# Kernel optimization log

Measured on AMD Instinct MI355X. Metric: run time of the kernel, lower is better.

## Reference

```python
import jax, jax.numpy as jnp
import numpy as np

FEAT_STRIDE = 16
PRE_NMS_TOPN = 6000
POST_NMS_TOPN = 300
NMS_THRESH = 0.7
MIN_SIZE = 16.0
NEG = -1e9


def _whctrs(a):
    w = a[2] - a[0] + 1.0
    h = a[3] - a[1] + 1.0
    return w, h, a[0] + 0.5 * (w - 1), a[1] + 0.5 * (h - 1)


def _mkanchors(ws, hs, xc, yc):
    return np.stack([xc - 0.5 * (ws - 1), yc - 0.5 * (hs - 1),
                     xc + 0.5 * (ws - 1), yc + 0.5 * (hs - 1)], axis=1)


def generate_anchors(base_size=16, ratios=(0.5, 1.0, 2.0), scales=(8, 16, 32)):
    base = np.array([0, 0, base_size - 1, base_size - 1], dtype=np.float64)
    w, h, xc, yc = _whctrs(base)
    size = w * h
    ratios = np.array(ratios, dtype=np.float64)
    ws = np.round(np.sqrt(size / ratios))
    hs = np.round(ws * ratios)
    ratio_anchors = _mkanchors(ws, hs, xc, yc)
    out = []
    for a in ratio_anchors:
        w, h, xc, yc = _whctrs(a)
        s = np.array(scales, dtype=np.float64)
        out.append(_mkanchors(w * s, h * s, xc, yc))
    return np.concatenate(out, axis=0).astype(np.float32)


def _nms_single(boxes, scores):
    # boxes [N,4], scores [N] (sorted desc by top_k); greedy NMS, fixed POST_NMS_TOPN picks
    x1, y1, x2, y2 = boxes[:, 0], boxes[:, 1], boxes[:, 2], boxes[:, 3]
    areas = (x2 - x1 + 1.0) * (y2 - y1 + 1.0)

    def body(i, st):
        keep, ok, live = st
        s = jnp.where(live, scores, NEG - 1.0)
        j = jnp.argmax(s)
        valid = s[j] > NEG / 2
        keep = keep.at[i].set(j.astype(jnp.int32))
        ok = ok.at[i].set(valid)
        xx1 = jnp.maximum(x1[j], x1)
        yy1 = jnp.maximum(y1[j], y1)
        xx2 = jnp.minimum(x2[j], x2)
        yy2 = jnp.minimum(y2[j], y2)
        inter = jnp.maximum(xx2 - xx1 + 1.0, 0.0) * jnp.maximum(yy2 - yy1 + 1.0, 0.0)
        iou = inter / (areas[j] + areas - inter)
        live = live & (iou <= NMS_THRESH)
        return keep, ok, live

    keep0 = jnp.zeros((POST_NMS_TOPN,), jnp.int32)
    ok0 = jnp.zeros((POST_NMS_TOPN,), bool)
    live0 = scores > NEG / 2
    keep, ok, _ = jax.lax.fori_loop(0, POST_NMS_TOPN, body, (keep0, ok0, live0))
    return keep, ok


def _proposals(rpn_cls_prob, rpn_bbox_pred, im_info, anchors):
    B, _, H, W = rpn_cls_prob.shape
    A = anchors.shape[0]
    # fg scores: second half of the 2A channel dim
    scores = rpn_cls_prob[:, A:].transpose(0, 2, 3, 1).reshape(B, -1)          # [B, H*W*A]
    deltas = rpn_bbox_pred.transpose(0, 2, 3, 1).reshape(B, -1, 4)             # [B, H*W*A, 4]
    # shifted anchors over the feature map
    sx = (jnp.arange(W, dtype=jnp.float32)) * FEAT_STRIDE
    sy = (jnp.arange(H, dtype=jnp.float32)) * FEAT_STRIDE
    gx, gy = jnp.meshgrid(sx, sy)                                              # [H, W]
    shifts = jnp.stack([gx.ravel(), gy.ravel(), gx.ravel(), gy.ravel()], 1)    # [K, 4]
    all_anchors = (shifts[:, None, :] + anchors[None, :, :]).reshape(-1, 4)    # [K*A, 4]
    # bbox_transform_inv
    wa = all_anchors[:, 2] - all_anchors[:, 0] + 1.0
    ha = all_anchors[:, 3] - all_anchors[:, 1] + 1.0
    cxa = all_anchors[:, 0] + 0.5 * (wa - 1.0)
    cya = all_anchors[:, 1] + 0.5 * (ha - 1.0)
    dx, dy, dw, dh = deltas[..., 0], deltas[..., 1], deltas[..., 2], deltas[..., 3]
    cx = dx * wa + cxa
    cy = dy * ha + cya
    pw = jnp.exp(dw) * wa
    ph = jnp.exp(dh) * ha
    x1 = cx - 0.5 * (pw - 1.0)
    y1 = cy - 0.5 * (ph - 1.0)
    x2 = cx + 0.5 * (pw - 1.0)
    y2 = cy + 0.5 * (ph - 1.0)
    # clip to image
    imh = im_info[:, 0:1]
    imw = im_info[:, 1:2]
    x1 = jnp.clip(x1, 0.0, imw - 1.0)
    y1 = jnp.clip(y1, 0.0, imh - 1.0)
    x2 = jnp.clip(x2, 0.0, imw - 1.0)
    y2 = jnp.clip(y2, 0.0, imh - 1.0)
    boxes = jnp.stack([x1, y1, x2, y2], axis=-1)                               # [B, N, 4]
    # filter boxes smaller than min_size * im_scale (mask by score)
    min_sz = MIN_SIZE * im_info[:, 2:3]
    keep_m = ((x2 - x1 + 1.0) >= min_sz) & ((y2 - y1 + 1.0) >= min_sz)
    scores = jnp.where(keep_m, scores, NEG)
    # pre-NMS top-k
    scores_top, order = jax.lax.top_k(scores, PRE_NMS_TOPN)                    # [B, 6000]
    boxes_top = jnp.take_along_axis(boxes, order[:, :, None], axis=1)          # [B, 6000, 4]
    # greedy NMS per image
    keep, keep_ok = jax.vmap(_nms_single)(boxes_top, scores_top)               # [B, 300]
    sel = jnp.take_along_axis(boxes_top, keep[:, :, None], axis=1)             # [B, 300, 4]
    sel = jnp.where(keep_ok[:, :, None], sel, 0.0)
    bidx = jnp.broadcast_to(jnp.arange(B, dtype=sel.dtype)[:, None, None], (B, POST_NMS_TOPN, 1))
    return jnp.concatenate([bidx, sel], axis=-1)                               # [B, 300, 5]


def setup_inputs() -> dict:
    key = jax.random.key(0)
    k1, k2 = jax.random.split(key)
    B, H, W, A = 32, 100, 100, 9
    rpn_cls_prob = jax.random.uniform(k1, (B, 2 * A, H, W), dtype=jnp.float32)
    rpn_bbox_pred = jax.random.normal(k2, (B, 4 * A, H, W), dtype=jnp.float32) * 0.2
    im_info = jnp.tile(jnp.array([[1600.0, 1600.0, 1.0]], dtype=jnp.float32), (B, 1))
    anchors = jnp.asarray(generate_anchors(base_size=16, ratios=(0.5, 1.0, 2.0), scales=(8, 16, 32)))
    return {"rpn_cls_prob": rpn_cls_prob, "rpn_bbox_pred": rpn_bbox_pred,
            "im_info": im_info, "anchors": anchors}


def reference(rpn_cls_prob, rpn_bbox_pred, im_info, anchors):
    return _proposals(rpn_cls_prob, rpn_bbox_pred, im_info, anchors)
```

## Files before the change

### kernel.cpp

```cpp
#include <hip/hip_runtime.h>

#define NB 32
#define NA 9
#define FH 100
#define FW 100
#define HWSZ (FH*FW)
#define NANCH (HWSZ*NA)
#define PRE 6000
#define POST 300
#define SORTN 8192
#define NEGV -1000000000.0f
#define NMS_T 0.7f
#define MARGM 1e-6f
#define NCHUNK ((PRE + 63) / 64)
#define WB() __builtin_amdgcn_wave_barrier()
#define NSLICE 11
#define DSLICE 8192

typedef unsigned long long u64;
typedef unsigned int u32;

__device__ __forceinline__ u32 f2sort(float f) {
  u32 u = __float_as_uint(f);
  return (u & 0x80000000u) ? ~u : (u | 0x80000000u);
}

__device__ __forceinline__ float4 decode_box_pm(const float* __restrict__ pred,
                                                const float* __restrict__ anchors,
                                                int b, int a, int hw,
                                                float imw, float imh) {
  int h = hw / FW; int w = hw - h * FW;
  float sx = (float)(w * 16);
  float sy = (float)(h * 16);
  float ax1 = anchors[a*4+0] + sx, ay1 = anchors[a*4+1] + sy;
  float ax2 = anchors[a*4+2] + sx, ay2 = anchors[a*4+3] + sy;
  float wa = ax2 - ax1 + 1.0f, ha = ay2 - ay1 + 1.0f;
  float cxa = ax1 + 0.5f*(wa - 1.0f), cya = ay1 + 0.5f*(ha - 1.0f);
  size_t base = ((size_t)b*36 + a*4)*HWSZ + hw;
  float dx = pred[base];
  float dy = pred[base + HWSZ];
  float dw = pred[base + 2*HWSZ];
  float dh = pred[base + 3*HWSZ];
  float cx = dx*wa + cxa, cy = dy*ha + cya;
  float pw = expf(dw)*wa, ph = expf(dh)*ha;
  float x1 = fminf(fmaxf(cx - 0.5f*(pw - 1.0f), 0.0f), imw - 1.0f);
  float y1 = fminf(fmaxf(cy - 0.5f*(ph - 1.0f), 0.0f), imh - 1.0f);
  float x2 = fminf(fmaxf(cx + 0.5f*(pw - 1.0f), 0.0f), imw - 1.0f);
  float y2 = fminf(fmaxf(cy + 0.5f*(ph - 1.0f), 0.0f), imh - 1.0f);
  return make_float4(x1, y1, x2, y2);
}

__global__ void k_zero(u32* __restrict__ histcnt) {
  int i = blockIdx.x * 1024 + threadIdx.x;
  histcnt[i] = 0;
}

__global__ __launch_bounds__(1024) void k_decode(
    const float* __restrict__ cls,
    const float* __restrict__ pred,
    const float* __restrict__ iminfo,
    const float* __restrict__ anchors,
    u32* __restrict__ scoreg,
    u32* __restrict__ histg) {
  __shared__ u32 hl[4096];
  const int blk = blockIdx.x;
  const int b = blk / NSLICE, s = blk - b * NSLICE;
  const int tid = threadIdx.x;
  for (int j = tid; j < 4096; j += 1024) hl[j] = 0;
  __syncthreads();
  const float imh = iminfo[b*3+0], imw = iminfo[b*3+1], sc = iminfo[b*3+2];
  const float msz = 16.0f * sc;
  #pragma unroll
  for (int r = 0; r < 8; ++r) {
    int j = s * DSLICE + r * 1024 + tid;
    if (j < NANCH) {
      int a = j / HWSZ; int hw = j - a * HWSZ;
      float score = cls[((size_t)b*18 + 9 + a)*HWSZ + hw];
      float4 bx = decode_box_pm(pred, anchors, b, a, hw, imw, imh);
      bool keep = ((bx.z - bx.x + 1.0f) >= msz) && ((bx.w - bx.y + 1.0f) >= msz);
      float sf = keep ? score : NEGV;
      float t = sf * 4096.0f;
      int bin = (t <= 0.0f) ? 0 : ((t >= 4095.0f) ? 4095 : (int)t);
      atomicAdd(&hl[bin], 1u);
      scoreg[(size_t)b * NANCH + j] = f2sort(sf);
    }
  }
  __syncthreads();
  for (int j = tid; j < 4096; j += 1024) {
    u32 v = hl[j];
    if (v) atomicAdd(&histg[b * 4096 + j], v);
  }
}

__device__ __forceinline__ void w0_cut(u32* hist, u32 target, int lane,
                                       int* cutBin) {
  u32 cs = 0;
  int cb = lane * 64;
  for (int i = 0; i < 64; ++i) cs += hist[cb + ((i + lane) & 63)];
  u32 suf = cs;
  #pragma unroll
  for (int d = 1; d < 64; d <<= 1) {
    u32 o = __shfl_down(suf, (unsigned)d, 64);
    suf += (lane < 64 - d) ? o : 0u;
  }
  u64 m1 = __ballot(suf >= target);
  int L = 63 - __clzll(m1);
  u32 nAb = (L < 63) ? (u32)__builtin_amdgcn_readlane((int)suf, L + 1) : 0u;
  u32 fs = hist[L * 64 + lane];
  #pragma unroll
  for (int d = 1; d < 64; d <<= 1) {
    u32 o = __shfl_down(fs, (unsigned)d, 64);
    fs += (lane < 64 - d) ? o : 0u;
  }
  fs += nAb;
  u64 m2 = __ballot(fs >= target);
  int fb = 63 - __clzll(m2);
  *cutBin = L * 64 + fb;
}

__global__ __launch_bounds__(64) void k_cut(const u32* __restrict__ histg,
                                            u32* __restrict__ thrTg,
                                            u32* __restrict__ binStartG,
                                            u32* __restrict__ countG) {
  __shared__ u32 hl[4096];
  const int b = blockIdx.x, lane = threadIdx.x;
  const u32* h = histg + b * 4096;
  for (int i = lane; i < 4096; i += 64) hl[i] = h[i];
  __syncthreads();
  int L;
  w0_cut(hl, PRE, lane, &L);
  u32 running = 0;
  for (int hi = 4095; hi >= L; hi -= 64) {
    int bin = hi - lane;
    u32 c = (bin >= L && bin >= 0) ? hl[bin] : 0u;
    u32 p = c;
    #pragma unroll
    for (int d = 1; d < 64; d <<= 1) {
      u32 o = __shfl_up(p, (unsigned)d, 64);
      if (lane >= d) p += o;
    }
    if (bin >= L && bin >= 0) binStartG[b * 4096 + bin] = running + p - c;
    running += (u32)__builtin_amdgcn_readlane((int)p, 63);
  }
  if (lane == 0) {
    thrTg[b] = f2sort((float)L * (1.0f / 4096.0f));
    countG[b] = running;
  }
}

__global__ __launch_bounds__(1024) void k_scatter(
    const u32* __restrict__ scoreg,
    const u32* __restrict__ thrTg,
    const u32* __restrict__ binStartG,
    u32* __restrict__ binCntG,
    u64* __restrict__ candg,
    float4* __restrict__ boxg,
    const float* __restrict__ pred,
    const float* __restrict__ iminfo,
    const float* __restrict__ anchors) {
  const int blk = blockIdx.x;
  const int b = blk / NSLICE, s = blk - b * NSLICE;
  const int tid = threadIdx.x;
  const u32 thrT = thrTg[b];
  const float imh = iminfo[b*3+0], imw = iminfo[b*3+1];
  const u32* sb = scoreg + (size_t)b * NANCH;
  #pragma unroll
  for (int r = 0; r < 8; ++r) {
    int j = s * DSLICE + r * 1024 + tid;
    if (j < NANCH) {
      u32 sv = sb[j];
      if (sv >= thrT) {
        int a = j / HWSZ; int hw = j - a * HWSZ;
        int i = hw * NA + a;
        float f = __uint_as_float(sv ^ 0x80000000u);
        float t = f * 4096.0f;
        int bin = (t >= 4095.0f) ? 4095 : (int)t;
        u32 pos = binStartG[b * 4096 + bin] + atomicAdd(&binCntG[b * 4096 + bin], 1u);
        if (pos < SORTN) {
          candg[(size_t)b * SORTN + pos] = ((u64)sv << 32) | (u32)(~(u32)i);
          boxg[(size_t)b * SORTN + pos] = decode_box_pm(pred, anchors, b, a, hw, imw, imh);
        }
      }
    }
  }
}

__global__ __launch_bounds__(512) void k_binsort(
    const u32* __restrict__ binStartG,
    const u32* __restrict__ binCntG,
    u64* __restrict__ candg,
    float4* __restrict__ boxg) {
  __shared__ u64 ks[8][512];
  __shared__ u32 ops[8][512];
  __shared__ float4 bs[8][512];
  const int wave = threadIdx.x >> 6, lane = threadIdx.x & 63;
  const int task = blockIdx.x * 8 + wave;
  const int b = task >> 12, bin = task & 4095;
  u32 cnt = binCntG[b * 4096 + bin];
  if (cnt < 2) return;
  u32 base = binStartG[b * 4096 + bin];
  if (base >= SORTN) return;
  u32 m = cnt;
  if (base + m > SORTN) m = SORTN - base;
  u64* seg = candg + (size_t)b * SORTN + base;
  float4* bseg = boxg + (size_t)b * SORTN + base;
  if (m <= 64) {
    u64 v = (lane < (int)m) ? seg[lane] : 0ull;
    u32 op = (u32)lane;
    #pragma unroll
    for (int k = 2; k <= 64; k <<= 1) {
      for (int j = k >> 1; j > 0; j >>= 1) {
        u64 o = __shfl_xor((unsigned long long)v, j, 64);
        u32 oop = __shfl_xor(op, j, 64);
        bool dirD = ((lane & k) == 0);
        bool lower = ((lane & j) == 0);
        bool takeMax = (dirD == lower);
        bool sw = takeMax ? (o > v) : (o < v);
        if (sw) { v = o; op = oop; }
      }
    }
    if (lane < (int)m) seg[lane] = v;
    if (lane < (int)m) {
      float4 bx = bseg[op];
      bseg[lane] = bx;
    }
  } else if (m <= 512) {
    int np = 128; while (np < (int)m) np <<= 1;
    for (int i = lane; i < np; i += 64) {
      ks[wave][i] = (i < (int)m) ? seg[i] : 0ull;
      ops[wave][i] = (u32)i;
    }
    WB();
    for (int k = 2; k <= np; k <<= 1) {
      for (int j = k >> 1; j > 0; j >>= 1) {
        for (int q = lane; q < np/2; q += 64) {
          int i = ((q & ~(j-1)) << 1) | (q & (j-1));
          int x = i | j;
          u64 a0 = ks[wave][i], a1 = ks[wave][x];
          bool up = (i & k) != 0;
          if (up ? (a0 > a1) : (a0 < a1)) {
            ks[wave][i] = a1; ks[wave][x] = a0;
            u32 t = ops[wave][i]; ops[wave][i] = ops[wave][x]; ops[wave][x] = t;
          }
        }
        WB();
      }
    }
    for (int i = lane; i < (int)m; i += 64) bs[wave][i] = bseg[ops[wave][i]];
    WB();
    for (int i = lane; i < (int)m; i += 64) {
      seg[i] = ks[wave][i];
      bseg[i] = bs[wave][i];
    }
  }
}

__global__ __launch_bounds__(512, 1) void k_nms(
    const float4* __restrict__ boxg,
    const u32* __restrict__ countG,
    float* __restrict__ out) {
  __shared__ float4 boxes[NCHUNK * 64];
  __shared__ float4 accB[POST];
  __shared__ float accA[POST];
  __shared__ u64 okm[2][8];
  const int b = blockIdx.x;
  const int tid = threadIdx.x;
  const int wave = tid >> 6, lane = tid & 63;
  int cnt = (int)countG[b]; if (cnt > PRE) cnt = PRE;
  const float4* bg = boxg + (size_t)b * SORTN;
  for (int i = tid; i < NCHUNK * 64; i += 512) boxes[i] = bg[i];
  __syncthreads();

  int nAcc = 0, lc = 0;
  for (int g = 0; g < NCHUNK; ++g) {
    if (nAcc >= POST) break;
    int nliv = cnt - g * 64;
    if (nliv <= 0) break;
    u64 lm = (nliv >= 64) ? ~0ull : ((1ull << nliv) - 1ull);
    float4 bc = boxes[g * 64 + lane];
    float areaC = (bc.z - bc.x + 1.0f) * (bc.w - bc.y + 1.0f);
    bool ok = (lm >> lane) & 1ull;
    for (int t0 = wave; t0 < nAcc; t0 += 128) {
      if (__ballot(ok) == 0ull) break;
      int te = (t0 + 128 < nAcc) ? (t0 + 128) : nAcc;
      #pragma unroll 2
      for (int tt = t0; tt < te; tt += 8) {
        float4 ba = accB[tt];
        float aA = accA[tt];
        float xx1 = fmaxf(ba.x, bc.x);
        float yy1 = fmaxf(ba.y, bc.y);
        float xx2 = fminf(ba.z, bc.z);
        float yy2 = fminf(ba.w, bc.w);
        float inter = fmaxf(xx2 - xx1 + 1.0f, 0.0f) * fmaxf(yy2 - yy1 + 1.0f, 0.0f);
        float un = aA + areaC - inter;
        float prod = NMS_T * un;
        bool sup = inter > prod;
        if (fabsf(inter - prod) <= MARGM * prod)
          sup = (inter / un) > NMS_T;
        ok = ok && !sup;
      }
    }
    u64 wm = __ballot(ok);
    if (lane == 0) okm[lc & 1][wave] = wm;
    __syncthreads();
    u64 mm = okm[lc & 1][0];
    #pragma unroll
    for (int w = 1; w < 8; ++w) mm &= okm[lc & 1][w];
    ++lc;
    bool ok0 = (mm >> lane) & 1ull;
    u64 bal = __ballot(ok0);
    while (bal != 0ull && nAcc < POST) {
      int fl = __ffsll(bal) - 1;
      float ax1 = __int_as_float(__builtin_amdgcn_readlane(__float_as_int(bc.x), fl));
      float ay1 = __int_as_float(__builtin_amdgcn_readlane(__float_as_int(bc.y), fl));
      float ax2 = __int_as_float(__builtin_amdgcn_readlane(__float_as_int(bc.z), fl));
      float ay2 = __int_as_float(__builtin_amdgcn_readlane(__float_as_int(bc.w), fl));
      float aA = (ax2 - ax1 + 1.0f) * (ay2 - ay1 + 1.0f);
      if (lane == 0) { accB[nAcc] = make_float4(ax1, ay1, ax2, ay2); accA[nAcc] = aA; }
      ++nAcc;
      if (ok0) {
        if (lane == fl) ok0 = false;
        else if (lane > fl) {
          float xx1 = fmaxf(ax1, bc.x);
          float yy1 = fmaxf(ay1, bc.y);
          float xx2 = fminf(ax2, bc.z);
          float yy2 = fminf(ay2, bc.w);
          float inter = fmaxf(xx2 - xx1 + 1.0f, 0.0f) * fmaxf(yy2 - yy1 + 1.0f, 0.0f);
          float iou = inter / (aA + areaC - inter);
          if (iou > NMS_T) ok0 = false;
        }
      }
      bal = __ballot(ok0);
    }
  }

  float* ob = out + (size_t)b * POST * 5;
  for (int i = tid; i < POST * 5; i += 512) {
    int row = i / 5, col = i - row * 5;
    float v = 0.f;
    if (col == 0) v = (float)b;
    else if (row < nAcc) {
      float4 bb = accB[row];
      v = (col == 1) ? bb.x : (col == 2) ? bb.y : (col == 3) ? bb.z : bb.w;
    }
    ob[i] = v;
  }
}

extern "C" void kernel_launch(void* const* d_in, const int* in_sizes, int n_in,
                              void* d_out, int out_size, void* d_ws, size_t ws_size,
                              hipStream_t stream) {
  const float* cls     = (const float*)d_in[0];
  const float* pred    = (const float*)d_in[1];
  const float* iminfo  = (const float*)d_in[2];
  const float* anchors = (const float*)d_in[3];
  float* out = (float*)d_out;

  char* ws = (char*)d_ws;
  u32* histg     = (u32*)(ws + 0);
  u32* binCntG   = (u32*)(ws + 524288);
  u32* binStartG = (u32*)(ws + 1048576);
  u32* thrTg     = (u32*)(ws + 1572864);
  u32* countG    = (u32*)(ws + 1572992);
  u64* candg     = (u64*)(ws + 1573120);
  float4* boxg   = (float4*)(ws + 3670272);
  u32* scoreg    = (u32*)(ws + 7864576);

  k_zero<<<256, 1024, 0, stream>>>(histg);
  k_decode<<<NB*NSLICE, 1024, 0, stream>>>(cls, pred, iminfo, anchors, scoreg, histg);
  k_cut<<<NB, 64, 0, stream>>>(histg, thrTg, binStartG, countG);
  k_scatter<<<NB*NSLICE, 1024, 0, stream>>>(scoreg, thrTg, binStartG, binCntG,
                                            candg, boxg, pred, iminfo, anchors);
  k_binsort<<<16384, 512, 0, stream>>>(binStartG, binCntG, candg, boxg);
  k_nms<<<NB, 512, 0, stream>>>(boxg, countG, out);
}
```

Baseline: 209.0 us.

## Widen NMS to 1024 threads with two candidate chunks per round and cheaper IoU test

The NMS kernel now uses 16 waves and handles two 64-candidate chunks per round, halving the number of block-wide synchronisation rounds. The suppression test is rewritten as a multiply-compare against precomputed 0.7*area terms, with an exact division only inside a narrow tolerance band. The zeroing kernel is replaced with a memset. The greedy accept loop now also has to check the second chunk against each newly accepted box, which adds serial work per round.

```diff
diff --git a/kernel.cpp b/kernel.cpp
--- a/kernel.cpp
+++ b/kernel.cpp
@@ -11,8 +11,9 @@
 #define SORTN 8192
 #define NEGV -1000000000.0f
 #define NMS_T 0.7f
-#define MARGM 1e-6f
+#define BANDR 4e-6f
 #define NCHUNK ((PRE + 63) / 64)
+#define NROUND 47
 #define WB() __builtin_amdgcn_wave_barrier()
 #define NSLICE 11
 #define DSLICE 8192
@@ -48,11 +49,6 @@
   float x2 = fminf(fmaxf(cx + 0.5f*(pw - 1.0f), 0.0f), imw - 1.0f);
   float y2 = fminf(fmaxf(cy + 0.5f*(ph - 1.0f), 0.0f), imh - 1.0f);
   return make_float4(x1, y1, x2, y2);
-}
-
-__global__ void k_zero(u32* __restrict__ histcnt) {
-  int i = blockIdx.x * 1024 + threadIdx.x;
-  histcnt[i] = 0;
 }
 
 __global__ __launch_bounds__(1024) void k_decode(
@@ -255,87 +251,155 @@
   }
 }
 
-__global__ __launch_bounds__(512, 1) void k_nms(
+__global__ __launch_bounds__(1024, 1) void k_nms(
     const float4* __restrict__ boxg,
     const u32* __restrict__ countG,
     float* __restrict__ out) {
   __shared__ float4 boxes[NCHUNK * 64];
   __shared__ float4 accB[POST];
-  __shared__ float accA[POST];
-  __shared__ u64 okm[2][8];
+  __shared__ float4 accT[POST];
+  __shared__ float accA7[POST];
+  __shared__ float accAr[POST];
+  __shared__ u64 okm[2][16][2];
   const int b = blockIdx.x;
   const int tid = threadIdx.x;
   const int wave = tid >> 6, lane = tid & 63;
   int cnt = (int)countG[b]; if (cnt > PRE) cnt = PRE;
   const float4* bg = boxg + (size_t)b * SORTN;
-  for (int i = tid; i < NCHUNK * 64; i += 512) boxes[i] = bg[i];
+  for (int i = tid; i < NCHUNK * 64; i += 1024) boxes[i] = bg[i];
   __syncthreads();
 
   int nAcc = 0, lc = 0;
-  for (int g = 0; g < NCHUNK; ++g) {
+  for (int g = 0; g < NROUND; ++g) {
     if (nAcc >= POST) break;
-    int nliv = cnt - g * 64;
+    int base0 = g * 128;
+    int nliv = cnt - base0;
     if (nliv <= 0) break;
-    u64 lm = (nliv >= 64) ? ~0ull : ((1ull << nliv) - 1ull);
-    float4 bc = boxes[g * 64 + lane];
-    float areaC = (bc.z - bc.x + 1.0f) * (bc.w - bc.y + 1.0f);
-    bool ok = (lm >> lane) & 1ull;
+    u64 lm0 = (nliv >= 64) ? ~0ull : ((1ull << nliv) - 1ull);
+    int nl1 = nliv - 64;
+    u64 lm1 = (nl1 >= 64) ? ~0ull : ((nl1 <= 0) ? 0ull : ((1ull << nl1) - 1ull));
+    float4 bc0 = boxes[base0 + lane];
+    float4 bc1 = boxes[base0 + 64 + lane];
+    float ar0 = (bc0.z - bc0.x + 1.0f) * (bc0.w - bc0.y + 1.0f);
+    float ar1 = (bc1.z - bc1.x + 1.0f) * (bc1.w - bc1.y + 1.0f);
+    float ca0 = NMS_T * ar0, ca1 = NMS_T * ar1;
+    float cz0 = bc0.z + 1.0f, cw0 = bc0.w + 1.0f;
+    float cz1 = bc1.z + 1.0f, cw1 = bc1.w + 1.0f;
+    bool ok0_ = (lm0 >> lane) & 1ull;
+    bool ok1_ = (lm1 >> lane) & 1ull;
     for (int t0 = wave; t0 < nAcc; t0 += 128) {
-      if (__ballot(ok) == 0ull) break;
+      if (__ballot(ok0_ || ok1_) == 0ull) break;
       int te = (t0 + 128 < nAcc) ? (t0 + 128) : nAcc;
-      #pragma unroll 2
-      for (int tt = t0; tt < te; tt += 8) {
-        float4 ba = accB[tt];
-        float aA = accA[tt];
-        float xx1 = fmaxf(ba.x, bc.x);
-        float yy1 = fmaxf(ba.y, bc.y);
-        float xx2 = fminf(ba.z, bc.z);
-        float yy2 = fminf(ba.w, bc.w);
-        float inter = fmaxf(xx2 - xx1 + 1.0f, 0.0f) * fmaxf(yy2 - yy1 + 1.0f, 0.0f);
-        float un = aA + areaC - inter;
-        float prod = NMS_T * un;
-        bool sup = inter > prod;
-        if (fabsf(inter - prod) <= MARGM * prod)
-          sup = (inter / un) > NMS_T;
-        ok = ok && !sup;
-      }
-    }
-    u64 wm = __ballot(ok);
-    if (lane == 0) okm[lc & 1][wave] = wm;
+      for (int tt = t0; tt < te; tt += 16) {
+        float4 bt = accT[tt];
+        float a7 = accA7[tt];
+        {
+          float xx1 = fmaxf(bt.x, bc0.x);
+          float yy1 = fmaxf(bt.y, bc0.y);
+          float x2p = fminf(bt.z, cz0);
+          float y2p = fminf(bt.w, cw0);
+          float inter = fmaxf(x2p - xx1, 0.0f) * fmaxf(y2p - yy1, 0.0f);
+          float lhs = 1.7f * inter;
+          float rhs = a7 + ca0;
+          bool sup = lhs > rhs;
+          if (fabsf(lhs - rhs) <= BANDR * rhs) {
+            float4 bo = accB[tt];
+            float xr1 = fmaxf(bo.x, bc0.x), yr1 = fmaxf(bo.y, bc0.y);
+            float xr2 = fminf(bo.z, bc0.z), yr2 = fminf(bo.w, bc0.w);
+            float ir = fmaxf(xr2 - xr1 + 1.0f, 0.0f) * fmaxf(yr2 - yr1 + 1.0f, 0.0f);
+            sup = (ir / (accAr[tt] + ar0 - ir)) > NMS_T;
+          }
+          ok0_ = ok0_ && !sup;
+        }
+        {
+          float xx1 = fmaxf(bt.x, bc1.x);
+          float yy1 = fmaxf(bt.y, bc1.y);
+          float x2p = fminf(bt.z, cz1);
+          float y2p = fminf(bt.w, cw1);
+          float inter = fmaxf(x2p - xx1, 0.0f) * fmaxf(y2p - yy1, 0.0f);
+          float lhs = 1.7f * inter;
+          float rhs = a7 + ca1;
+          bool sup = lhs > rhs;
+          if (fabsf(lhs - rhs) <= BANDR * rhs) {
+            float4 bo = accB[tt];
+            float xr1 = fmaxf(bo.x, bc1.x), yr1 = fmaxf(bo.y, bc1.y);
+            float xr2 = fminf(bo.z, bc1.z), yr2 = fminf(bo.w, bc1.w);
+            float ir = fmaxf(xr2 - xr1 + 1.0f, 0.0f) * fmaxf(yr2 - yr1 + 1.0f, 0.0f);
+            sup = (ir / (accAr[tt] + ar1 - ir)) > NMS_T;
+          }
+          ok1_ = ok1_ && !sup;
+        }
+      }
+    }
+    u64 w0 = __ballot(ok0_);
+    u64 w1 = __ballot(ok1_);
+    if (lane == 0) { okm[lc & 1][wave][0] = w0; okm[lc & 1][wave][1] = w1; }
     __syncthreads();
-    u64 mm = okm[lc & 1][0];
+    u64 m0 = okm[lc & 1][0][0], m1 = okm[lc & 1][0][1];
     #pragma unroll
-    for (int w = 1; w < 8; ++w) mm &= okm[lc & 1][w];
+    for (int w = 1; w < 16; ++w) { m0 &= okm[lc & 1][w][0]; m1 &= okm[lc & 1][w][1]; }
     ++lc;
-    bool ok0 = (mm >> lane) & 1ull;
-    u64 bal = __ballot(ok0);
-    while (bal != 0ull && nAcc < POST) {
-      int fl = __ffsll(bal) - 1;
-      float ax1 = __int_as_float(__builtin_amdgcn_readlane(__float_as_int(bc.x), fl));
-      float ay1 = __int_as_float(__builtin_amdgcn_readlane(__float_as_int(bc.y), fl));
-      float ax2 = __int_as_float(__builtin_amdgcn_readlane(__float_as_int(bc.z), fl));
-      float ay2 = __int_as_float(__builtin_amdgcn_readlane(__float_as_int(bc.w), fl));
+    bool k0 = (m0 >> lane) & 1ull;
+    bool k1 = (m1 >> lane) & 1ull;
+    u64 bal0 = __ballot(k0), bal1 = __ballot(k1);
+    while ((bal0 | bal1) != 0ull && nAcc < POST) {
+      bool from0 = (bal0 != 0ull);
+      float ax1, ay1, ax2, ay2;
+      int fl;
+      if (from0) {
+        fl = __ffsll(bal0) - 1;
+        ax1 = __int_as_float(__builtin_amdgcn_readlane(__float_as_int(bc0.x), fl));
+        ay1 = __int_as_float(__builtin_amdgcn_readlane(__float_as_int(bc0.y), fl));
+        ax2 = __int_as_float(__builtin_amdgcn_readlane(__float_as_int(bc0.z), fl));
+        ay2 = __int_as_float(__builtin_amdgcn_readlane(__float_as_int(bc0.w), fl));
+      } else {
+        fl = __ffsll(bal1) - 1;
+        ax1 = __int_as_float(__builtin_amdgcn_readlane(__float_as_int(bc1.x), fl));
+        ay1 = __int_as_float(__builtin_amdgcn_readlane(__float_as_int(bc1.y), fl));
+        ax2 = __int_as_float(__builtin_amdgcn_readlane(__float_as_int(bc1.z), fl));
+        ay2 = __int_as_float(__builtin_amdgcn_readlane(__float_as_int(bc1.w), fl));
+      }
       float aA = (ax2 - ax1 + 1.0f) * (ay2 - ay1 + 1.0f);
-      if (lane == 0) { accB[nAcc] = make_float4(ax1, ay1, ax2, ay2); accA[nAcc] = aA; }
+      if (lane == 0) {
+        accB[nAcc] = make_float4(ax1, ay1, ax2, ay2);
+        accT[nAcc] = make_float4(ax1, ay1, ax2 + 1.0f, ay2 + 1.0f);
+        accA7[nAcc] = NMS_T * aA;
+        accAr[nAcc] = aA;
+      }
       ++nAcc;
-      if (ok0) {
-        if (lane == fl) ok0 = false;
-        else if (lane > fl) {
-          float xx1 = fmaxf(ax1, bc.x);
-          float yy1 = fmaxf(ay1, bc.y);
-          float xx2 = fminf(ax2, bc.z);
-          float yy2 = fminf(ay2, bc.w);
+      if (from0) {
+        if (k0) {
+          if (lane == fl) k0 = false;
+          else if (lane > fl) {
+            float xx1 = fmaxf(ax1, bc0.x), yy1 = fmaxf(ay1, bc0.y);
+            float xx2 = fminf(ax2, bc0.z), yy2 = fminf(ay2, bc0.w);
+            float inter = fmaxf(xx2 - xx1 + 1.0f, 0.0f) * fmaxf(yy2 - yy1 + 1.0f, 0.0f);
+            if (inter / (aA + ar0 - inter) > NMS_T) k0 = false;
+          }
+        }
+        if (k1) {
+          float xx1 = fmaxf(ax1, bc1.x), yy1 = fmaxf(ay1, bc1.y);
+          float xx2 = fminf(ax2, bc1.z), yy2 = fminf(ay2, bc1.w);
           float inter = fmaxf(xx2 - xx1 + 1.0f, 0.0f) * fmaxf(yy2 - yy1 + 1.0f, 0.0f);
-          float iou = inter / (aA + areaC - inter);
-          if (iou > NMS_T) ok0 = false;
-        }
-      }
-      bal = __ballot(ok0);
+          if (inter / (aA + ar1 - inter) > NMS_T) k1 = false;
+        }
+      } else {
+        if (k1) {
+          if (lane == fl) k1 = false;
+          else if (lane > fl) {
+            float xx1 = fmaxf(ax1, bc1.x), yy1 = fmaxf(ay1, bc1.y);
+            float xx2 = fminf(ax2, bc1.z), yy2 = fminf(ay2, bc1.w);
+            float inter = fmaxf(xx2 - xx1 + 1.0f, 0.0f) * fmaxf(yy2 - yy1 + 1.0f, 0.0f);
+            if (inter / (aA + ar1 - inter) > NMS_T) k1 = false;
+          }
+        }
+      }
+      bal0 = __ballot(k0); bal1 = __ballot(k1);
     }
   }
 
   float* ob = out + (size_t)b * POST * 5;
-  for (int i = tid; i < POST * 5; i += 512) {
+  for (int i = tid; i < POST * 5; i += 1024) {
     int row = i / 5, col = i - row * 5;
     float v = 0.f;
     if (col == 0) v = (float)b;
@@ -366,11 +430,11 @@
   float4* boxg   = (float4*)(ws + 3670272);
   u32* scoreg    = (u32*)(ws + 7864576);
 
-  k_zero<<<256, 1024, 0, stream>>>(histg);
+  hipMemsetAsync(ws, 0, 1048576, stream);
   k_decode<<<NB*NSLICE, 1024, 0, stream>>>(cls, pred, iminfo, anchors, scoreg, histg);
   k_cut<<<NB, 64, 0, stream>>>(histg, thrTg, binStartG, countG);
   k_scatter<<<NB*NSLICE, 1024, 0, stream>>>(scoreg, thrTg, binStartG, binCntG,
                                             candg, boxg, pred, iminfo, anchors);
   k_binsort<<<16384, 512, 0, stream>>>(binStartG, binCntG, candg, boxg);
-  k_nms<<<NB, 512, 0, stream>>>(boxg, countG, out);
-}
+  k_nms<<<NB, 1024, 0, stream>>>(boxg, countG, out);
+}
```

Measured after the change: 300.2 us. 43.6% more time.
